# Performance work log

Measured on AMD Instinct MI355X. Metric: run time of the kernel, lower is better.

The kernel has to match this reference:

```python
import jax, jax.numpy as jnp
import numpy as np

# Product-key memory config (matches init_kwargs)
HEADS = 4
K_DIM = 512          # per-head query/key dim; split in two halves of 256
HALF = K_DIM // 2
V_DIM = 512
SUBSIZE = 512        # sub-keys per bank; value table size = SUBSIZE**2
SIZE = SUBSIZE * SUBSIZE
TOPK = 8
TEMP = 1.0
B, T = 4, 2048


def setup_inputs() -> dict:
    key = jax.random.key(0)
    kq, kk, kv = jax.random.split(key, 3)
    bound = 1.0 / np.sqrt(K_DIM)  # reset_parameters: uniform(-1/sqrt(k_dim), 1/sqrt(k_dim))
    query = jax.random.normal(kq, (B, T, HEADS * K_DIM), dtype=jnp.float32)
    keys = jax.random.uniform(kk, (2 * HEADS * SUBSIZE, HALF), dtype=jnp.float32,
                              minval=-bound, maxval=bound)
    # reset_parameters: normal(0, v_dim**-0.5)
    values = jax.random.normal(kv, (SIZE, V_DIM), dtype=jnp.float32) * (V_DIM ** -0.5)
    return {"query": query, "keys": keys, "values": values}


def reference(query, keys, values):
    """retrieve_values: product-key two-stage topk + softmax-weighted embedding bag.
    query: [B, T, HEADS*K_DIM]; keys: [2*HEADS*SUBSIZE, HALF]; values: [SIZE, V_DIM]
    returns retrieved values [B*T, V_DIM].
    """
    Bq, Tq = query.shape[:2]
    N = Bq * Tq
    q = query.reshape(N, HEADS, K_DIM)
    q1, q2 = q[..., :HALF], q[..., HALF:]
    k = keys.reshape(2, HEADS, SUBSIZE, HALF)

    # Sub-key score matmuls (the two 'cdist-like' searches)
    s1 = jnp.einsum('nhd,hsd->nhs', q1, k[0])       # [N, H, SUBSIZE]
    s2 = jnp.einsum('nhd,hsd->nhs', q2, k[1])       # [N, H, SUBSIZE]

    ts1, ti1 = jax.lax.top_k(s1, TOPK)               # [N, H, TOPK]
    ts2, ti2 = jax.lax.top_k(s2, TOPK)

    # Cartesian combination of the two topk sets, then global topk
    comb = (ts1[..., :, None] + ts2[..., None, :]).reshape(N, HEADS, TOPK * TOPK)
    scores, flat_idx = jax.lax.top_k(comb, TOPK)     # [N, H, TOPK]
    sel1 = jnp.take_along_axis(ti1, flat_idx // TOPK, axis=-1)
    sel2 = jnp.take_along_axis(ti2, flat_idx % TOPK, axis=-1)
    indices = sel1 * SUBSIZE + sel2                  # global value-table indices [N, H, TOPK]

    # score_transform: softmax over heads*topk (score_nonlinear='softmax')
    w = jax.nn.softmax(scores.reshape(N, HEADS * TOPK) / TEMP, axis=-1)

    # xformers_embedding_bag: weighted gather-sum over the huge value table
    gathered = values[indices.reshape(N, HEADS * TOPK)]   # [N, H*TOPK, V_DIM]
    vals = jnp.einsum('nk,nkd->nd', w, gathered)          # [N, V_DIM]
    return vals
```

## Files before the change

kernel.cpp:

```cpp
#include <hip/hip_runtime.h>
#include <hip/hip_bf16.h>
#include <math.h>

typedef unsigned short u16;
typedef __attribute__((ext_vector_type(8))) short short8;
typedef __attribute__((ext_vector_type(4))) float f32x4;

#define N_TOK   8192
#define N_HEADS 4
#define KDIM    512
#define HALFD   256
#define VDIM    512
#define SUBK    512
#define NCAND   16

__device__ __forceinline__ u16 f2bf(float f) {
    unsigned u = __float_as_uint(f);
    u += 0x7fffu + ((u >> 16) & 1u);
    return (u16)(u >> 16);
}

__global__ void k_convert(const float* __restrict__ in, u16* __restrict__ out, int n4) {
    int i = blockIdx.x * blockDim.x + threadIdx.x;
    int stride = gridDim.x * blockDim.x;
    for (; i < n4; i += stride) {
        float4 v = ((const float4*)in)[i];
        unsigned a = (unsigned)f2bf(v.x) | ((unsigned)f2bf(v.y) << 16);
        unsigned b = (unsigned)f2bf(v.z) | ((unsigned)f2bf(v.w) << 16);
        ((uint2*)out)[i] = make_uint2(a, b);
    }
}

__global__ __launch_bounds__(256) void k_score_topk(
    const u16* __restrict__ qb,
    const u16* __restrict__ kb,
    int* __restrict__ cand)
{
    __shared__ float sc[16 * 513];
    const int nb = blockIdx.x, h = blockIdx.y, half = blockIdx.z;
    const int tid = threadIdx.x;
    const int wave = tid >> 6, l = tid & 63;
    const int lr = l & 15, lk = l >> 4;

    const u16* qbase = qb + (size_t)(nb * 16 + lr) * (N_HEADS * KDIM) + h * KDIM + half * HALFD + lk * 8;
    short8 a[8];
#pragma unroll
    for (int kf = 0; kf < 8; ++kf)
        a[kf] = *(const short8*)(qbase + kf * 32);

    const u16* kbase = kb + (size_t)(half * N_HEADS + h) * SUBK * HALFD;
    for (int t = 0; t < 8; ++t) {
        int st = wave * 8 + t;
        const u16* kp = kbase + (size_t)(st * 16 + lr) * HALFD + lk * 8;
        short8 b[8];
#pragma unroll
        for (int kf = 0; kf < 8; ++kf)
            b[kf] = *(const short8*)(kp + kf * 32);
        f32x4 acc = {0.f, 0.f, 0.f, 0.f};
#pragma unroll
        for (int kf = 0; kf < 8; ++kf)
            acc = __builtin_amdgcn_mfma_f32_16x16x32_bf16(a[kf], b[kf], acc, 0, 0, 0);
#pragma unroll
        for (int r = 0; r < 4; ++r)
            sc[(lk * 4 + r) * 513 + st * 16 + lr] = acc[r];
    }
    __syncthreads();

    const int row = tid >> 4, sub = tid & 15;
    float tv[NCAND]; int ti[NCAND];
#pragma unroll
    for (int j = 0; j < NCAND; ++j) { tv[j] = -3e38f; ti[j] = 0; }
    for (int t = 0; t < 32; ++t) {
        int s = sub + (t << 4);
        float v = sc[row * 513 + s];
        if (v > tv[NCAND - 1]) {
#pragma unroll
            for (int j = NCAND - 1; j >= 0; --j) {
                bool cj = v > tv[j];
                bool cm = (j > 0) ? (v > tv[j - 1]) : false;
                float pv = (j > 0) ? tv[j - 1] : 0.f;
                int   pi = (j > 0) ? ti[j - 1] : 0;
                float nv = cj ? (cm ? pv : v) : tv[j];
                int   ni = cj ? (cm ? pi : s) : ti[j];
                tv[j] = nv; ti[j] = ni;
            }
        }
    }

    int keepidx = 0;
    for (int r = 0; r < NCAND; ++r) {
        float m = tv[0]; int mi = ti[0]; int ml = sub;
#pragma unroll
        for (int d = 1; d < 16; d <<= 1) {
            float ov = __shfl_xor(m, d, 16);
            int   oi = __shfl_xor(mi, d, 16);
            int   ol = __shfl_xor(ml, d, 16);
            if (ov > m || (ov == m && ol < ml)) { m = ov; mi = oi; ml = ol; }
        }
        if (sub == r) keepidx = mi;
        if (ml == sub) {
#pragma unroll
            for (int j = 0; j < NCAND - 1; ++j) { tv[j] = tv[j + 1]; ti[j] = ti[j + 1]; }
            tv[NCAND - 1] = -3e38f;
        }
    }
    int n = nb * 16 + row;
    cand[((size_t)n * 8 + (h * 2 + half)) * NCAND + sub] = keepidx;
}

__global__ __launch_bounds__(256) void k_select(
    const float* __restrict__ query,
    const float* __restrict__ keys,
    const int* __restrict__ cand,
    int* __restrict__ gout,
    float* __restrict__ wout)
{
    __shared__ double rv[8][16];
    __shared__ int    ri[8][16];
    __shared__ double tsv[8][8];
    __shared__ int    tsi[8][8];
    __shared__ double s_comb[32];
    __shared__ int    sgi[32];

    const int n = blockIdx.x;
    const int tid = threadIdx.x;

    {
        const int dot = tid >> 1, part = tid & 1;
        const int g = dot >> 4, j = dot & 15;
        const int h = g >> 1, half = g & 1;
        const int sidx = cand[((size_t)n * 8 + g) * NCAND + j];
        const float* qrow = query + (size_t)n * (N_HEADS * KDIM) + h * KDIM + half * HALFD + part * 128;
        const float* krow = keys + ((size_t)(half * N_HEADS + h) * SUBK + sidx) * HALFD + part * 128;
        double a0 = 0, a1 = 0, a2 = 0, a3 = 0;
#pragma unroll 8
        for (int d = 0; d < 128; d += 4) {
            float4 qv = *(const float4*)(qrow + d);
            float4 kv = *(const float4*)(krow + d);
            a0 = fma((double)qv.x, (double)kv.x, a0);
            a1 = fma((double)qv.y, (double)kv.y, a1);
            a2 = fma((double)qv.z, (double)kv.z, a2);
            a3 = fma((double)qv.w, (double)kv.w, a3);
        }
        double s = (a0 + a1) + (a2 + a3);
        double o = __shfl_xor(s, 1);
        if (part == 0) { rv[g][j] = s + o; ri[g][j] = sidx; }
    }
    __syncthreads();

    if (tid < 128) {
        const int g = tid >> 4, j = tid & 15;
        double v = rv[g][j];
        const int idx = ri[g][j];
        for (int r = 0; r < 8; ++r) {
            double bv = v; int bj = j;
#pragma unroll
            for (int d = 1; d < 16; d <<= 1) {
                double ov = __shfl_xor(bv, d, 16);
                int    oj = __shfl_xor(bj, d, 16);
                if (ov > bv || (ov == bv && oj < bj)) { bv = ov; bj = oj; }
            }
            int widx = __shfl(idx, bj, 16);
            if (j == r) { tsv[g][r] = bv; tsi[g][r] = widx; }
            if (j == bj) v = -1e300;
        }
    }
    __syncthreads();

    {
        const int h = tid >> 6, f = tid & 63;
        double c = tsv[h * 2][f >> 3] + tsv[h * 2 + 1][f & 7];
        for (int r = 0; r < 8; ++r) {
            double bv = c; int bf = f;
#pragma unroll
            for (int d = 1; d < 64; d <<= 1) {
                double ov = __shfl_xor(bv, d, 64);
                int    of = __shfl_xor(bf, d, 64);
                if (ov > bv || (ov == bv && of < bf)) { bv = ov; bf = of; }
            }
            if (f == r) {
                s_comb[h * 8 + r] = bv;
                sgi[h * 8 + r] = tsi[h * 2][bf >> 3] * SUBK + tsi[h * 2 + 1][bf & 7];
            }
            if (f == bf) c = -1e300;
        }
    }
    __syncthreads();

    if (tid < 32) {
        const int k = tid;
        double s = s_comb[k];
        double m = s;
#pragma unroll
        for (int d = 1; d < 32; d <<= 1) m = fmax(m, __shfl_xor(m, d, 32));
        float e = expf((float)(s - m));
        float sum = e;
#pragma unroll
        for (int d = 1; d < 32; d <<= 1) sum += __shfl_xor(sum, d, 32);
        wout[(size_t)n * 32 + k] = e / sum;
        gout[(size_t)n * 32 + k] = sgi[k];
    }
}

__global__ __launch_bounds__(256) void k_gather(
    const float* __restrict__ values,
    const int* __restrict__ gidx,
    const float* __restrict__ w,
    float* __restrict__ out)
{
    __shared__ float  ws_[32];
    __shared__ size_t off_[32];
    const int n = blockIdx.x;
    const int tid = threadIdx.x;
    if (tid < 32) {
        ws_[tid] = w[(size_t)n * 32 + tid];
        off_[tid] = (size_t)gidx[(size_t)n * 32 + tid] * VDIM;
    }
    __syncthreads();

    float a0 = 0.f, a1 = 0.f;
#pragma unroll
    for (int kb = 0; kb < 32; kb += 16) {
        float2 v[16];
#pragma unroll
        for (int k = 0; k < 16; ++k)
            v[k] = ((const float2*)(values + off_[kb + k]))[tid];
#pragma unroll
        for (int k = 0; k < 16; ++k) {
            float wk = ws_[kb + k];
            a0 = fmaf(wk, v[k].x, a0);
            a1 = fmaf(wk, v[k].y, a1);
        }
    }
    ((float2*)(out + (size_t)n * VDIM))[tid] = make_float2(a0, a1);
}

extern "C" void kernel_launch(void* const* d_in, const int* in_sizes, int n_in,
                              void* d_out, int out_size, void* d_ws, size_t ws_size,
                              hipStream_t stream) {
    const float* query  = (const float*)d_in[0];
    const float* keys   = (const float*)d_in[1];
    const float* values = (const float*)d_in[2];
    float* out = (float*)d_out;

    char* ws = (char*)d_ws;
    u16* qb    = (u16*)ws;
    u16* kb    = (u16*)(ws + 33554432);
    int* cand  = (int*)(ws + 33554432 + 2097152);
    int* gidxb = (int*)(ws + 33554432 + 2097152 + 4194304);
    float* wb  = (float*)(ws + 33554432 + 2097152 + 4194304 + 1048576);

    k_convert<<<4096, 256, 0, stream>>>(query, qb, (N_TOK * N_HEADS * KDIM) / 4);
    k_convert<<<512, 256, 0, stream>>>(keys, kb, (2 * N_HEADS * SUBK * HALFD) / 4);

    dim3 gB(N_TOK / 16, N_HEADS, 2);
    k_score_topk<<<gB, 256, 0, stream>>>(qb, kb, cand);

    k_select<<<N_TOK, 256, 0, stream>>>(query, keys, cand, gidxb, wb);
    k_gather<<<N_TOK, 256, 0, stream>>>(values, gidxb, wb, out);
}
```

Before: 427.3 us.

## Fuse query bf16 conversion into scoring and use packed-key med3 top-k

Drops the separate query-to-bf16 conversion kernel and its 32MB workspace round trip by converting fp32 query values inline in the scoring kernel. Scores are packed into order-preserving unsigned keys with the column index in the low 9 bits, so the per-thread top-16 insertion becomes a branch-free v_med3_u32 network and the cross-lane merge becomes plain unsigned max. The gather kernel issues all 32 row loads at once with 32-bit offsets. Truncating the low 9 mantissa bits of scores only changes which candidates are kept in near-ties, and the exact fp64 rescoring in k_select still ranks the final set. The cost is more registers per thread.

```diff
diff --git a/kernel.cpp b/kernel.cpp
--- a/kernel.cpp
+++ b/kernel.cpp
@@ -18,6 +18,12 @@
     unsigned u = __float_as_uint(f);
     u += 0x7fffu + ((u >> 16) & 1u);
     return (u16)(u >> 16);
+}
+
+__device__ __forceinline__ unsigned med3u(unsigned a, unsigned b, unsigned c) {
+    unsigned d;
+    asm("v_med3_u32 %0, %1, %2, %3" : "=v"(d) : "v"(a), "v"(b), "v"(c));
+    return d;
 }
 
 __global__ void k_convert(const float* __restrict__ in, u16* __restrict__ out, int n4) {
@@ -32,25 +38,35 @@
 }
 
 __global__ __launch_bounds__(256) void k_score_topk(
-    const u16* __restrict__ qb,
+    const float* __restrict__ query,
     const u16* __restrict__ kb,
     int* __restrict__ cand)
 {
-    __shared__ float sc[16 * 513];
+    __shared__ unsigned sc[16 * 513];
     const int nb = blockIdx.x, h = blockIdx.y, half = blockIdx.z;
     const int tid = threadIdx.x;
     const int wave = tid >> 6, l = tid & 63;
     const int lr = l & 15, lk = l >> 4;
 
-    const u16* qbase = qb + (size_t)(nb * 16 + lr) * (N_HEADS * KDIM) + h * KDIM + half * HALFD + lk * 8;
+    const float* qbase = query + (size_t)(nb * 16 + lr) * (N_HEADS * KDIM)
+                       + h * KDIM + half * HALFD + lk * 8;
     short8 a[8];
 #pragma unroll
-    for (int kf = 0; kf < 8; ++kf)
-        a[kf] = *(const short8*)(qbase + kf * 32);
+    for (int kf = 0; kf < 8; ++kf) {
+        float4 q0 = *(const float4*)(qbase + kf * 32);
+        float4 q1 = *(const float4*)(qbase + kf * 32 + 4);
+        short8 t;
+        t[0] = (short)f2bf(q0.x); t[1] = (short)f2bf(q0.y);
+        t[2] = (short)f2bf(q0.z); t[3] = (short)f2bf(q0.w);
+        t[4] = (short)f2bf(q1.x); t[5] = (short)f2bf(q1.y);
+        t[6] = (short)f2bf(q1.z); t[7] = (short)f2bf(q1.w);
+        a[kf] = t;
+    }
 
     const u16* kbase = kb + (size_t)(half * N_HEADS + h) * SUBK * HALFD;
+#pragma unroll
     for (int t = 0; t < 8; ++t) {
-        int st = wave * 8 + t;
+        const int st = wave * 8 + t;
         const u16* kp = kbase + (size_t)(st * 16 + lr) * HALFD + lk * 8;
         short8 b[8];
 #pragma unroll
@@ -61,51 +77,46 @@
         for (int kf = 0; kf < 8; ++kf)
             acc = __builtin_amdgcn_mfma_f32_16x16x32_bf16(a[kf], b[kf], acc, 0, 0, 0);
 #pragma unroll
-        for (int r = 0; r < 4; ++r)
-            sc[(lk * 4 + r) * 513 + st * 16 + lr] = acc[r];
+        for (int r = 0; r < 4; ++r) {
+            unsigned ub = __float_as_uint(acc[r]);
+            unsigned key = ub ^ ((unsigned)((int)ub >> 31) | 0x80000000u);
+            key = (key & 0xFFFFFE00u) | (unsigned)(st * 16 + lr);
+            sc[(lk * 4 + r) * 513 + st * 16 + lr] = key;
+        }
     }
     __syncthreads();
 
     const int row = tid >> 4, sub = tid & 15;
-    float tv[NCAND]; int ti[NCAND];
-#pragma unroll
-    for (int j = 0; j < NCAND; ++j) { tv[j] = -3e38f; ti[j] = 0; }
+    unsigned tv[NCAND];
+#pragma unroll
+    for (int j = 0; j < NCAND; ++j) tv[j] = 0u;
+    const int base = row * 513 + sub;
+#pragma unroll
     for (int t = 0; t < 32; ++t) {
-        int s = sub + (t << 4);
-        float v = sc[row * 513 + s];
-        if (v > tv[NCAND - 1]) {
-#pragma unroll
-            for (int j = NCAND - 1; j >= 0; --j) {
-                bool cj = v > tv[j];
-                bool cm = (j > 0) ? (v > tv[j - 1]) : false;
-                float pv = (j > 0) ? tv[j - 1] : 0.f;
-                int   pi = (j > 0) ? ti[j - 1] : 0;
-                float nv = cj ? (cm ? pv : v) : tv[j];
-                int   ni = cj ? (cm ? pi : s) : ti[j];
-                tv[j] = nv; ti[j] = ni;
-            }
-        }
-    }
-
-    int keepidx = 0;
+        unsigned v = sc[base + (t << 4)];
+#pragma unroll
+        for (int j = NCAND - 1; j >= 1; --j)
+            tv[j] = med3u(tv[j - 1], tv[j], v);
+        tv[0] = (tv[0] > v) ? tv[0] : v;
+    }
+
+    unsigned keep = 0;
+#pragma unroll
     for (int r = 0; r < NCAND; ++r) {
-        float m = tv[0]; int mi = ti[0]; int ml = sub;
+        unsigned w = tv[0];
 #pragma unroll
         for (int d = 1; d < 16; d <<= 1) {
-            float ov = __shfl_xor(m, d, 16);
-            int   oi = __shfl_xor(mi, d, 16);
-            int   ol = __shfl_xor(ml, d, 16);
-            if (ov > m || (ov == m && ol < ml)) { m = ov; mi = oi; ml = ol; }
-        }
-        if (sub == r) keepidx = mi;
-        if (ml == sub) {
-#pragma unroll
-            for (int j = 0; j < NCAND - 1; ++j) { tv[j] = tv[j + 1]; ti[j] = ti[j + 1]; }
-            tv[NCAND - 1] = -3e38f;
-        }
-    }
-    int n = nb * 16 + row;
-    cand[((size_t)n * 8 + (h * 2 + half)) * NCAND + sub] = keepidx;
+            unsigned o = __shfl_xor(w, d, 16);
+            w = (o > w) ? o : w;
+        }
+        if (sub == r) keep = w;
+        bool pop = (tv[0] == w);
+#pragma unroll
+        for (int j = 0; j < NCAND - 1; ++j) tv[j] = pop ? tv[j + 1] : tv[j];
+        tv[NCAND - 1] = pop ? 0u : tv[NCAND - 1];
+    }
+    const int n = nb * 16 + row;
+    cand[((size_t)n * 8 + (h * 2 + half)) * NCAND + sub] = (int)(keep & 0x1FFu);
 }
 
 __global__ __launch_bounds__(256) void k_select(
@@ -208,29 +219,28 @@
     const float* __restrict__ w,
     float* __restrict__ out)
 {
-    __shared__ float  ws_[32];
-    __shared__ size_t off_[32];
+    __shared__ float    ws_[32];
+    __shared__ unsigned off2_[32];
     const int n = blockIdx.x;
     const int tid = threadIdx.x;
     if (tid < 32) {
         ws_[tid] = w[(size_t)n * 32 + tid];
-        off_[tid] = (size_t)gidx[(size_t)n * 32 + tid] * VDIM;
-    }
-    __syncthreads();
+        off2_[tid] = (unsigned)gidx[(size_t)n * 32 + tid] * 256u;
+    }
+    __syncthreads();
+
+    const float2* v2 = (const float2*)values;
+    float2 v[32];
+#pragma unroll
+    for (int k = 0; k < 32; ++k)
+        v[k] = v2[(size_t)off2_[k] + (unsigned)tid];
 
     float a0 = 0.f, a1 = 0.f;
 #pragma unroll
-    for (int kb = 0; kb < 32; kb += 16) {
-        float2 v[16];
-#pragma unroll
-        for (int k = 0; k < 16; ++k)
-            v[k] = ((const float2*)(values + off_[kb + k]))[tid];
-#pragma unroll
-        for (int k = 0; k < 16; ++k) {
-            float wk = ws_[kb + k];
-            a0 = fmaf(wk, v[k].x, a0);
-            a1 = fmaf(wk, v[k].y, a1);
-        }
+    for (int k = 0; k < 32; ++k) {
+        float wk = ws_[k];
+        a0 = fmaf(wk, v[k].x, a0);
+        a1 = fmaf(wk, v[k].y, a1);
     }
     ((float2*)(out + (size_t)n * VDIM))[tid] = make_float2(a0, a1);
 }
@@ -244,17 +254,15 @@
     float* out = (float*)d_out;
 
     char* ws = (char*)d_ws;
-    u16* qb    = (u16*)ws;
-    u16* kb    = (u16*)(ws + 33554432);
-    int* cand  = (int*)(ws + 33554432 + 2097152);
-    int* gidxb = (int*)(ws + 33554432 + 2097152 + 4194304);
-    float* wb  = (float*)(ws + 33554432 + 2097152 + 4194304 + 1048576);
-
-    k_convert<<<4096, 256, 0, stream>>>(query, qb, (N_TOK * N_HEADS * KDIM) / 4);
+    u16* kb    = (u16*)ws;
+    int* cand  = (int*)(ws + 2097152);
+    int* gidxb = (int*)(ws + 2097152 + 4194304);
+    float* wb  = (float*)(ws + 2097152 + 4194304 + 1048576);
+
     k_convert<<<512, 256, 0, stream>>>(keys, kb, (2 * N_HEADS * SUBK * HALFD) / 4);
 
     dim3 gB(N_TOK / 16, N_HEADS, 2);
-    k_score_topk<<<gB, 256, 0, stream>>>(qb, kb, cand);
+    k_score_topk<<<gB, 256, 0, stream>>>(query, kb, cand);
 
     k_select<<<N_TOK, 256, 0, stream>>>(query, keys, cand, gidxb, wb);
     k_gather<<<N_TOK, 256, 0, stream>>>(values, gidxb, wb, out);
```

After: 409.6 us. 1.04x faster.
